# Kernel tuning notes

Hardware: AMD Instinct MI355X
Metric: run time of the kernel (lower is better)

The kernel has to match this reference:

```python
import jax, jax.numpy as jnp
import numpy as np

B, C_IN, N, C_OUT, K = 16, 64, 2048, 64, 20
BN_EPS = 1e-5
SLOPE = 0.2  # LeakyReLU negative slope


def setup_inputs() -> dict:
    key = jax.random.key(0)
    ks = jax.random.split(key, 6)
    x = jax.random.normal(ks[0], (B, C_IN, N), jnp.float32)
    # Conv2d(2*C_IN, C_OUT, 1, bias=False), kaiming-normal init -> [C_OUT, 2*C_IN]
    W = jax.random.normal(ks[1], (C_OUT, 2 * C_IN), jnp.float32) * np.sqrt(2.0 / (2 * C_IN))
    # BatchNorm2d (eval mode) affine params + running stats
    gamma = jax.random.uniform(ks[2], (C_OUT,), jnp.float32, 0.5, 1.5)
    beta = jax.random.normal(ks[3], (C_OUT,), jnp.float32) * 0.1
    run_mean = jax.random.normal(ks[4], (C_OUT,), jnp.float32) * 0.1
    run_var = jax.random.uniform(ks[5], (C_OUT,), jnp.float32, 0.5, 1.5)
    return {"x": x, "W": W, "gamma": gamma, "beta": beta,
            "run_mean": run_mean, "run_var": run_var}


def _knn(x):
    """x: [B, C, N] -> neighbor indices [B, N, K] (nearest, includes self)."""
    xt = jnp.swapaxes(x, 1, 2)                       # [B, N, C]
    sq = jnp.sum(xt * xt, axis=-1)                   # [B, N]
    # squared euclidean distance; topk of -dist == nearest neighbors
    dist = sq[:, :, None] - 2.0 * jnp.einsum('bnc,bmc->bnm', xt, xt) + sq[:, None, :]
    _, idx = jax.lax.top_k(-dist, K)                 # [B, N, K]
    return idx


def reference(x, W, gamma, beta, run_mean, run_var):
    # --- dynamic graph (knn computed under no_grad in the original) ---
    idx = _knn(jax.lax.stop_gradient(x))             # [B, N, K]
    # --- dual gather: edge_index[1]=neighbors -> x_i, edge_index[0]=centers -> x_j ---
    xt = jnp.swapaxes(x, 1, 2)                       # [B, N, C]
    x_i = jax.vmap(lambda xb, ib: xb[ib])(xt, idx)   # [B, N, K, C] neighbor feats
    x_i = jnp.transpose(x_i, (0, 3, 1, 2))           # [B, C, N, K]
    x_j = x[:, :, :, None]                           # [B, C, N, 1] center feats
    feat = jnp.concatenate([x_i, x_j - x_i], axis=1)  # [B, 2C, N, K]
    # --- 1x1 conv (no bias) ---
    h = jnp.einsum('oc,bcnk->bonk', W, feat)         # [B, C_OUT, N, K]
    # --- BatchNorm2d eval mode, folded affine ---
    inv = gamma / jnp.sqrt(run_var + BN_EPS)
    h = h * inv[None, :, None, None] + (beta - run_mean * inv)[None, :, None, None]
    # --- LeakyReLU(0.2); Dropout(0.0) is identity ---
    h = jnp.where(h > 0, h, SLOPE * h)
    # --- max over neighbors ---
    out = jnp.max(h, axis=-1)                        # [B, C_OUT, N]
    return out, idx
```

## Files before the change

kernel.cpp:

```cpp
#include <hip/hip_runtime.h>
#include <cstdint>
#include <cstddef>

#define B_ 16
#define C_ 64
#define N_ 2048
#define K_ 20
#define CAND 24
#define LQ 12

typedef short bf16x8 __attribute__((ext_vector_type(8)));
typedef float f32x4 __attribute__((ext_vector_type(4)));

__device__ __forceinline__ unsigned umin_(unsigned a, unsigned b) { return a < b ? a : b; }
__device__ __forceinline__ unsigned umax_(unsigned a, unsigned b) { return a > b ? a : b; }
__device__ __forceinline__ unsigned short bfr_(float v) {
    unsigned u = __float_as_uint(v);
    return (unsigned short)((u + 0x7FFFu + ((u >> 16) & 1u)) >> 16);
}

__global__ __launch_bounds__(128) void k_sq(const float* __restrict__ x,
                                            float* __restrict__ sqf,
                                            unsigned short* __restrict__ xh,
                                            float* __restrict__ xrT,
                                            float* __restrict__ Yt,
                                            const float* __restrict__ W) {
    __shared__ float Ag[C_ * 64];
    int tid = threadIdx.x;
    bool doY = (Yt != nullptr);
    if (doY) {
        int o = tid & 63, ch = tid >> 6;
#pragma unroll
        for (int j = 0; j < 32; ++j) {
            int c = ch * 32 + j;
            Ag[c * 64 + o] = W[o * 128 + c] - W[o * 128 + 64 + c];
        }
    }
    int i = blockIdx.x * 128 + tid;
    int b = i >> 11, n = i & (N_ - 1);
    const float* xb = x + (size_t)b * C_ * N_ + n;
    float vr[C_];
#pragma unroll
    for (int c = 0; c < C_; ++c) vr[c] = xb[(size_t)c * N_];
    float p[C_];
#pragma unroll
    for (int c = 0; c < C_; ++c) p[c] = __fmul_rn(vr[c], vr[c]);
    float r[8];
#pragma unroll
    for (int k = 0; k < 8; ++k) r[k] = p[k];
#pragma unroll
    for (int ii = 8; ii < 64; ii += 8) {
#pragma unroll
        for (int k = 0; k < 8; ++k) r[k] = __fadd_rn(r[k], p[ii + k]);
    }
    float s0 = __fadd_rn(__fadd_rn(r[0], r[1]), __fadd_rn(r[2], r[3]));
    float s1 = __fadd_rn(__fadd_rn(r[4], r[5]), __fadd_rn(r[6], r[7]));
    sqf[i] = __fadd_rn(s0, s1);

    unsigned short* xrow = xh + (size_t)i * 64;
#pragma unroll
    for (int cb = 0; cb < 8; ++cb) {
        bf16x8 pk;
#pragma unroll
        for (int e = 0; e < 8; ++e) pk[e] = (short)bfr_(vr[cb * 8 + e]);
        *reinterpret_cast<bf16x8*>(xrow + ((cb ^ (n & 7)) * 8)) = pk;
    }
    if (xrT) {
        float4* dst = reinterpret_cast<float4*>(xrT + (size_t)i * C_);
#pragma unroll
        for (int q = 0; q < 16; ++q)
            dst[q] = make_float4(vr[q*4+0], vr[q*4+1], vr[q*4+2], vr[q*4+3]);
    }
    if (doY) {
        __syncthreads();
        float4 acc[16];
#pragma unroll
        for (int q = 0; q < 16; ++q) acc[q] = make_float4(0.f, 0.f, 0.f, 0.f);
#pragma unroll 4
        for (int c = 0; c < C_; ++c) {
            float xv = vr[c];
            const float4* a4 = reinterpret_cast<const float4*>(&Ag[c * 64]);
#pragma unroll
            for (int q = 0; q < 16; ++q) {
                float4 a = a4[q];
                acc[q].x = fmaf(xv, a.x, acc[q].x);
                acc[q].y = fmaf(xv, a.y, acc[q].y);
                acc[q].z = fmaf(xv, a.z, acc[q].z);
                acc[q].w = fmaf(xv, a.w, acc[q].w);
            }
        }
        float4* yp = reinterpret_cast<float4*>(Yt + (size_t)i * 64);
#pragma unroll
        for (int q = 0; q < 16; ++q) yp[q] = acc[q];
    }
}

__global__ __launch_bounds__(256) void k_y(const float* __restrict__ x,
                                           const float* __restrict__ W,
                                           float* __restrict__ Yt) {
    __shared__ float Al[C_ * 64];
    __shared__ float xl[C_ * 64];
    int tid = threadIdx.x;
    int bid = blockIdx.x;
    int b = bid >> 5;
    int m0 = (bid & 31) * 64;
    {
        int o = tid & 63, cb = tid >> 6;
#pragma unroll
        for (int j = 0; j < 16; ++j) {
            int c = cb * 16 + j;
            Al[c * 64 + o] = W[o * 128 + c] - W[o * 128 + 64 + c];
            xl[c * 64 + o] = x[((size_t)b * C_ + c) * N_ + m0 + o];
        }
    }
    __syncthreads();
    int ml = tid & 63, og = tid >> 6;
    float acc[16];
#pragma unroll
    for (int j = 0; j < 16; ++j) acc[j] = 0.f;
#pragma unroll 4
    for (int c = 0; c < C_; ++c) {
        float xv = xl[c * 64 + ml];
        const float4* a4 = reinterpret_cast<const float4*>(&Al[c * 64 + og * 16]);
#pragma unroll
        for (int q = 0; q < 4; ++q) {
            float4 av = a4[q];
            acc[q*4+0] = fmaf(av.x, xv, acc[q*4+0]);
            acc[q*4+1] = fmaf(av.y, xv, acc[q*4+1]);
            acc[q*4+2] = fmaf(av.z, xv, acc[q*4+2]);
            acc[q*4+3] = fmaf(av.w, xv, acc[q*4+3]);
        }
    }
    float* yp = Yt + ((size_t)b * N_ + m0 + ml) * C_ + og * 16;
#pragma unroll
    for (int q = 0; q < 4; ++q)
        reinterpret_cast<float4*>(yp)[q] =
            make_float4(acc[q*4+0], acc[q*4+1], acc[q*4+2], acc[q*4+3]);
}

__global__ __launch_bounds__(256, 2) void k_dist(const unsigned short* __restrict__ xh,
                                                 const float* __restrict__ sqf,
                                                 unsigned short* __restrict__ candu) {
    __shared__ __align__(16) unsigned short xtl[256 * 64];
    __shared__ float sqm[256];
    int tid = threadIdx.x;
    int w = tid >> 6, lane = tid & 63;
    int bid = blockIdx.x;
    int b = bid >> 5;
    int n0 = (bid & 31) * 64;
    const unsigned short* xhb = xh + (size_t)b * N_ * 64;

    {
#pragma unroll
        for (int i = 0; i < 2; ++i) {
            int ch = tid + 256 * i;
            *reinterpret_cast<uint4*>(&xtl[ch * 8]) =
                *reinterpret_cast<const uint4*>(&xhb[(size_t)n0 * 64 + ch * 8]);
        }
    }
    __syncthreads();
    int rl = w * 16 + (lane & 15);
    int cb0 = (lane >> 4), cb1 = 4 + (lane >> 4);
    bf16x8 afr0 = *reinterpret_cast<const bf16x8*>(&xtl[rl * 64 + ((cb0 ^ (lane & 7)) * 8)]);
    bf16x8 afr1 = *reinterpret_cast<const bf16x8*>(&xtl[rl * 64 + ((cb1 ^ (lane & 7)) * 8)]);
    float rsq[4];
#pragma unroll
    for (int r = 0; r < 4; ++r)
        rsq[r] = sqf[b * N_ + n0 + w * 16 + (lane >> 4) * 4 + r];

    unsigned list[4][LQ];
#pragma unroll
    for (int r = 0; r < 4; ++r)
#pragma unroll
        for (int j = 0; j < LQ; ++j) list[r][j] = 0xFFFFFFFFu;

    for (int t = 0; t < 8; ++t) {
        int m0 = t * 256;
        __syncthreads();
        {
#pragma unroll
            for (int i = 0; i < 8; ++i) {
                int ch = tid + 256 * i;
                *reinterpret_cast<uint4*>(&xtl[ch * 8]) =
                    *reinterpret_cast<const uint4*>(&xhb[(size_t)m0 * 64 + ch * 8]);
            }
            sqm[tid] = sqf[b * N_ + m0 + tid];
        }
        __syncthreads();
        const unsigned short* pB0 = &xtl[(lane & 15) * 64 + ((cb0 ^ (lane & 7)) * 8)];
        const unsigned short* pB1 = &xtl[(lane & 15) * 64 + ((cb1 ^ (lane & 7)) * 8)];
        const float* pS = &sqm[lane & 15];
#pragma unroll
        for (int mb = 0; mb < 16; ++mb) {
            bf16x8 bf0 = *reinterpret_cast<const bf16x8*>(pB0 + mb * 1024);
            bf16x8 bf1 = *reinterpret_cast<const bf16x8*>(pB1 + mb * 1024);
            f32x4 acc = {0.f, 0.f, 0.f, 0.f};
            acc = __builtin_amdgcn_mfma_f32_16x16x32_bf16(afr0, bf0, acc, 0, 0, 0);
            acc = __builtin_amdgcn_mfma_f32_16x16x32_bf16(afr1, bf1, acc, 0, 0, 0);
            float smv = pS[mb * 16];
            unsigned mg = (unsigned)(m0 + mb * 16) | (unsigned)(lane & 15);
#pragma unroll
            for (int r = 0; r < 4; ++r) {
                float rs = rsq[r] + smv;
                float d = fmaf(-2.f, acc[r], rs);
                d = fmaxf(d, 0.f);
                unsigned key = (__float_as_uint(d) & 0xFFFFF800u) | mg;
#pragma unroll
                for (int j = LQ - 1; j > 0; --j)
                    asm("v_med3_u32 %0, %0, %1, %2"
                        : "+v"(list[r][j])
                        : "v"(list[r][j - 1]), "v"(key));
                list[r][0] = umin_(list[r][0], key);
            }
        }
    }

    size_t grow0 = (size_t)b * N_ + n0 + w * 16 + (lane >> 4) * 4;
#pragma unroll 1
    for (int it = 0; it < CAND; ++it) {
        unsigned head[4], wv[4];
#pragma unroll
        for (int j = 0; j < 4; ++j) { head[j] = list[j][0]; wv[j] = head[j]; }
#pragma unroll
        for (int d2 = 1; d2 < 16; d2 <<= 1)
#pragma unroll
            for (int j = 0; j < 4; ++j)
                wv[j] = umin_(wv[j], (unsigned)__shfl_xor((int)wv[j], d2, 16));
#pragma unroll
        for (int j = 0; j < 4; ++j) {
            bool own = (head[j] == wv[j]);
#pragma unroll
            for (int jj = 0; jj < LQ - 1; ++jj)
                list[j][jj] = own ? list[j][jj + 1] : list[j][jj];
            list[j][LQ - 1] = own ? 0xFFFFFFFFu : list[j][LQ - 1];
            if ((lane & 15) == 0)
                candu[(grow0 + j) * CAND + it] = (unsigned short)(wv[j] & 2047u);
        }
    }
}

__global__ __launch_bounds__(256) void k_rescore2(const float* __restrict__ xrT,
                                                  const float* __restrict__ sqf,
                                                  const unsigned short* __restrict__ candu,
                                                  float* __restrict__ idxf) {
    __shared__ __align__(16) float xnl[64 * 64];
    __shared__ unsigned short cl[64 * CAND];
    __shared__ float dl2[64][CAND];
    int tid = threadIdx.x;
    int bid = blockIdx.x;
    int b = bid >> 5;
    int n0 = (bid & 31) * 64;
    int bN = b * N_;
    const float* xr = xrT + (size_t)bN * C_;
    {
        const float4* src = reinterpret_cast<const float4*>(xr + (size_t)n0 * C_);
#pragma unroll
        for (int q = 0; q < 4; ++q) {
            int idx = tid + q * 256;
            reinterpret_cast<float4*>(xnl)[idx] = src[idx];
        }
        if (tid < 192) {
            reinterpret_cast<uint4*>(cl)[tid] =
                reinterpret_cast<const uint4*>(candu + (size_t)(bN + n0) * CAND)[tid];
        }
    }
    __syncthreads();
#pragma unroll 1
    for (int t2 = 0; t2 < 6; ++t2) {
        int task = tid + t2 * 256;
        int row = task / 24, ci = task - row * 24;
        int m = cl[row * CAND + ci];
        const float* xn = xnl + row * 64;
        const float* xm = xr + (size_t)m * C_;
        float a = 0.f;
#pragma unroll
        for (int cq = 0; cq < 16; ++cq) {
            float4 n4 = *reinterpret_cast<const float4*>(xn + cq * 4);
            float4 m4 = *reinterpret_cast<const float4*>(xm + cq * 4);
            a = __fadd_rn(a, __fmul_rn(n4.x, m4.x));
            a = __fadd_rn(a, __fmul_rn(n4.y, m4.y));
            a = __fadd_rn(a, __fmul_rn(n4.z, m4.z));
            a = __fadd_rn(a, __fmul_rn(n4.w, m4.w));
        }
        dl2[row][ci] = __fadd_rn(__fsub_rn(sqf[bN + n0 + row], __fmul_rn(2.0f, a)),
                                 sqf[bN + m]);
    }
    __syncthreads();
#pragma unroll 1
    for (int t2 = 0; t2 < 6; ++t2) {
        int task = tid + t2 * 256;
        int row = task / 24, ci = task - row * 24;
        int m = cl[row * CAND + ci];
        float di = dl2[row][ci];
        int rank = 0;
#pragma unroll
        for (int j = 0; j < CAND; ++j) {
            float dj = dl2[row][j];
            int mj = cl[row * CAND + j];
            rank += (dj < di || (dj == di && mj < m)) ? 1 : 0;
        }
        if (rank < K_)
            idxf[((size_t)bN + n0 + row) * K_ + rank] = (float)m;
    }
}

__global__ __launch_bounds__(256) void k_rescore(const float* __restrict__ x,
                                                 const float* __restrict__ sqf,
                                                 const unsigned short* __restrict__ candu,
                                                 float* __restrict__ idxf) {
    int tid = threadIdx.x;
    int w = tid >> 6, lane = tid & 63;
    size_t grow = (size_t)blockIdx.x * 4 + w;
    int b = (int)(grow >> 11), n = (int)(grow & (N_ - 1));
    const float* xb = x + (size_t)b * C_ * N_;
    float d = 0.f;
    unsigned m = 0xFFFFFFFFu;
    if (lane < CAND) {
        m = candu[grow * CAND + lane];
        float a = 0.f;
#pragma unroll 8
        for (int c = 0; c < C_; ++c)
            a = __fadd_rn(a, __fmul_rn(xb[(size_t)c * N_ + n], xb[(size_t)c * N_ + m]));
        d = __fadd_rn(__fsub_rn(sqf[b * N_ + n], __fmul_rn(2.0f, a)), sqf[b * N_ + m]);
    }
    int rank = 0;
#pragma unroll 1
    for (int j = 0; j < CAND; ++j) {
        float dj = __shfl(d, j, 64);
        unsigned mj = (unsigned)__shfl((int)m, j, 64);
        if (lane < CAND && (dj < d || (dj == d && mj < m))) ++rank;
    }
    if (lane < CAND && rank < K_)
        idxf[grow * K_ + rank] = (float)m;
}

__global__ __launch_bounds__(256) void k_out(const float* __restrict__ x,
                                             const float* __restrict__ W,
                                             const float* __restrict__ gamma,
                                             const float* __restrict__ beta,
                                             const float* __restrict__ rmean,
                                             const float* __restrict__ rvar,
                                             const float* __restrict__ Yt,
                                             const float* __restrict__ idxf,
                                             float* __restrict__ out) {
    __shared__ float Bl[C_ * 64];
    __shared__ float xl[C_ * 64];
    __shared__ float resl[64 * 65];
    __shared__ float sl[64], tl[64];
    int tid = threadIdx.x;
    int bid = blockIdx.x;
    int b = bid >> 5;
    int n0 = (bid & 31) * 64;
    {
        int o = tid & 63, cb = tid >> 6;
#pragma unroll
        for (int j = 0; j < 16; ++j) {
            int c = cb * 16 + j;
            Bl[c * 64 + o] = W[o * 128 + 64 + c];
            xl[c * 64 + o] = x[((size_t)b * C_ + c) * N_ + n0 + o];
        }
        if (tid < 64) {
            float s = gamma[tid] / sqrtf(rvar[tid] + 1e-5f);
            sl[tid] = s;
            tl[tid] = beta[tid] - rmean[tid] * s;
        }
    }
    __syncthreads();
    int nl = tid & 63, wv2 = tid >> 6;
    const float* ip = idxf + ((size_t)b * N_ + n0 + nl) * K_;
    int mi[K_];
#pragma unroll
    for (int k = 0; k < K_; ++k) mi[k] = (int)ip[k];
    const float* Ytb = Yt + (size_t)b * N_ * C_;
#pragma unroll
    for (int t = 0; t < 4; ++t) {
        int oq = wv2 * 4 + t;
        float ax = 0.f, ay = 0.f, az = 0.f, aw = 0.f;
#pragma unroll 8
        for (int c = 0; c < C_; ++c) {
            float xv = xl[c * 64 + nl];
            float4 bl4 = *reinterpret_cast<const float4*>(&Bl[c * 64 + oq * 4]);
            ax = fmaf(bl4.x, xv, ax);
            ay = fmaf(bl4.y, xv, ay);
            az = fmaf(bl4.z, xv, az);
            aw = fmaf(bl4.w, xv, aw);
        }
        float vx = -3.4e38f, vy = -3.4e38f, vz = -3.4e38f, vw = -3.4e38f;
#pragma unroll
        for (int k = 0; k < K_; ++k) {
            float4 y4 = *reinterpret_cast<const float4*>(&Ytb[(size_t)mi[k] * C_ + oq * 4]);
            vx = fmaxf(vx, y4.x);
            vy = fmaxf(vy, y4.y);
            vz = fmaxf(vz, y4.z);
            vw = fmaxf(vw, y4.w);
        }
        float h0 = ax + vx, h1 = ay + vy, h2 = az + vz, h3 = aw + vw;
        int o0 = oq * 4;
        float v0 = sl[o0 + 0] * h0 + tl[o0 + 0];
        float v1 = sl[o0 + 1] * h1 + tl[o0 + 1];
        float v2 = sl[o0 + 2] * h2 + tl[o0 + 2];
        float v3 = sl[o0 + 3] * h3 + tl[o0 + 3];
        v0 = v0 > 0.f ? v0 : 0.2f * v0;
        v1 = v1 > 0.f ? v1 : 0.2f * v1;
        v2 = v2 > 0.f ? v2 : 0.2f * v2;
        v3 = v3 > 0.f ? v3 : 0.2f * v3;
        resl[(o0 + 0) * 65 + nl] = v0;
        resl[(o0 + 1) * 65 + nl] = v1;
        resl[(o0 + 2) * 65 + nl] = v2;
        resl[(o0 + 3) * 65 + nl] = v3;
    }
    __syncthreads();
    {
        int nl2 = tid & 63, ob = tid >> 6;
#pragma unroll
        for (int j = 0; j < 16; ++j) {
            int o2 = ob * 16 + j;
            out[((size_t)b * C_ + o2) * N_ + n0 + nl2] = resl[o2 * 65 + nl2];
        }
    }
}

extern "C" void kernel_launch(void* const* d_in, const int* in_sizes, int n_in,
                              void* d_out, int out_size, void* d_ws, size_t ws_size,
                              hipStream_t stream) {
    const float* x     = (const float*)d_in[0];
    const float* W     = (const float*)d_in[1];
    const float* gamma = (const float*)d_in[2];
    const float* beta  = (const float*)d_in[3];
    const float* rmean = (const float*)d_in[4];
    const float* rvar  = (const float*)d_in[5];

    float* out  = (float*)d_out;
    float* idxf = out + (size_t)B_ * C_ * N_;

    char* ws = (char*)d_ws;
    float* sqf            = (float*)ws;
    unsigned short* candu = (unsigned short*)(ws + 131072);
    unsigned short* xh    = (unsigned short*)(ws + 131072 + 1572864);
    size_t off_xrT        = 131072 + 1572864 + 4194304;
    size_t need_xrT       = off_xrT + 8388608;
    size_t need_fused     = need_xrT + 8388608;
    float* xrT            = (ws_size >= need_xrT) ? (float*)(ws + off_xrT) : nullptr;
    bool fused            = (ws_size >= need_fused);
    float* Yt             = fused ? (float*)(ws + need_xrT) : (float*)(ws + 131072);

    k_sq     <<<B_ * N_ / 128, 128, 0, stream>>>(x, sqf, xh, xrT, fused ? Yt : nullptr, W);
    k_dist   <<<B_ * 32, 256, 0, stream>>>(xh, sqf, candu);
    if (xrT)
        k_rescore2<<<B_ * 32, 256, 0, stream>>>(xrT, sqf, candu, idxf);
    else
        k_rescore<<<B_ * N_ / 4, 256, 0, stream>>>(x, sqf, candu, idxf);
    if (!fused)
        k_y  <<<B_ * (N_ / 64), 256, 0, stream>>>(x, W, Yt);
    k_out    <<<B_ * (N_ / 64), 256, 0, stream>>>(x, W, gamma, beta, rmean, rvar, Yt, idxf, out);
}
```

Baseline: 178.5 us.

## Coalesce rescore candidate loads via shuffles, unfuse Y, per-channel gather in k_out

The Y projection is moved out of k_sq and always computed by the separate k_y kernel, which lightens k_sq. k_rescore3 assigns each group of four lanes to four candidate rows: each lane loads a 16-float slice of every row and the slices are redistributed with wave shuffles, so candidate-row reads are contiguous instead of one 256-byte row per lane. k_out stages neighbour indices in shared memory and gathers Y with one output channel per lane, giving coalesced 64-float row reads instead of scattered float4 reads. The cost is many shuffle instructions, an extra kernel launch, and extra synchronisation in k_out.

```diff
diff --git a/kernel.cpp b/kernel.cpp
--- a/kernel.cpp
+++ b/kernel.cpp
@@ -22,20 +22,8 @@
 __global__ __launch_bounds__(128) void k_sq(const float* __restrict__ x,
                                             float* __restrict__ sqf,
                                             unsigned short* __restrict__ xh,
-                                            float* __restrict__ xrT,
-                                            float* __restrict__ Yt,
-                                            const float* __restrict__ W) {
-    __shared__ float Ag[C_ * 64];
-    int tid = threadIdx.x;
-    bool doY = (Yt != nullptr);
-    if (doY) {
-        int o = tid & 63, ch = tid >> 6;
-#pragma unroll
-        for (int j = 0; j < 32; ++j) {
-            int c = ch * 32 + j;
-            Ag[c * 64 + o] = W[o * 128 + c] - W[o * 128 + 64 + c];
-        }
-    }
+                                            float* __restrict__ xrT) {
+    int tid = threadIdx.x;
     int i = blockIdx.x * 128 + tid;
     int b = i >> 11, n = i & (N_ - 1);
     const float* xb = x + (size_t)b * C_ * N_ + n;
@@ -70,28 +58,6 @@
 #pragma unroll
         for (int q = 0; q < 16; ++q)
             dst[q] = make_float4(vr[q*4+0], vr[q*4+1], vr[q*4+2], vr[q*4+3]);
-    }
-    if (doY) {
-        __syncthreads();
-        float4 acc[16];
-#pragma unroll
-        for (int q = 0; q < 16; ++q) acc[q] = make_float4(0.f, 0.f, 0.f, 0.f);
-#pragma unroll 4
-        for (int c = 0; c < C_; ++c) {
-            float xv = vr[c];
-            const float4* a4 = reinterpret_cast<const float4*>(&Ag[c * 64]);
-#pragma unroll
-            for (int q = 0; q < 16; ++q) {
-                float4 a = a4[q];
-                acc[q].x = fmaf(xv, a.x, acc[q].x);
-                acc[q].y = fmaf(xv, a.y, acc[q].y);
-                acc[q].z = fmaf(xv, a.z, acc[q].z);
-                acc[q].w = fmaf(xv, a.w, acc[q].w);
-            }
-        }
-        float4* yp = reinterpret_cast<float4*>(Yt + (size_t)i * 64);
-#pragma unroll
-        for (int q = 0; q < 16; ++q) yp[q] = acc[q];
     }
 }
 
@@ -239,7 +205,7 @@
     }
 }
 
-__global__ __launch_bounds__(256) void k_rescore2(const float* __restrict__ xrT,
+__global__ __launch_bounds__(256) void k_rescore3(const float* __restrict__ xrT,
                                                   const float* __restrict__ sqf,
                                                   const unsigned short* __restrict__ candu,
                                                   float* __restrict__ idxf) {
@@ -247,6 +213,7 @@
     __shared__ unsigned short cl[64 * CAND];
     __shared__ float dl2[64][CAND];
     int tid = threadIdx.x;
+    int lane = tid & 63, w = tid >> 6;
     int bid = blockIdx.x;
     int b = bid >> 5;
     int n0 = (bid & 31) * 64;
@@ -259,24 +226,59 @@
             int idx = tid + q * 256;
             reinterpret_cast<float4*>(xnl)[idx] = src[idx];
         }
-        if (tid < 192) {
+        if (tid < 192)
             reinterpret_cast<uint4*>(cl)[tid] =
                 reinterpret_cast<const uint4*>(candu + (size_t)(bN + n0) * CAND)[tid];
-        }
-    }
-    __syncthreads();
+    }
+    __syncthreads();
+    int qbase = lane & ~3, qr = lane & 3;
 #pragma unroll 1
-    for (int t2 = 0; t2 < 6; ++t2) {
-        int task = tid + t2 * 256;
-        int row = task / 24, ci = task - row * 24;
+    for (int s = 0; s < 6; ++s) {
+        int task = w * 384 + s * 64 + lane;
+        int row = task / CAND, ci = task - row * CAND;
         int m = cl[row * CAND + ci];
+        float4 buf[16];
+#pragma unroll
+        for (int r = 0; r < 4; ++r) {
+            int mq = __shfl(m, qbase + r, 64);
+            const float* xmq = xr + (size_t)mq * C_ + qr * 16;
+            float4 c0 = *reinterpret_cast<const float4*>(xmq + 0);
+            float4 c1 = *reinterpret_cast<const float4*>(xmq + 4);
+            float4 c2 = *reinterpret_cast<const float4*>(xmq + 8);
+            float4 c3 = *reinterpret_cast<const float4*>(xmq + 12);
+#pragma unroll
+            for (int j2 = 0; j2 < 4; ++j2) {
+                float4 s0, s1, s2, s3;
+                s0.x = __shfl(c0.x, qbase + j2, 64);
+                s0.y = __shfl(c0.y, qbase + j2, 64);
+                s0.z = __shfl(c0.z, qbase + j2, 64);
+                s0.w = __shfl(c0.w, qbase + j2, 64);
+                s1.x = __shfl(c1.x, qbase + j2, 64);
+                s1.y = __shfl(c1.y, qbase + j2, 64);
+                s1.z = __shfl(c1.z, qbase + j2, 64);
+                s1.w = __shfl(c1.w, qbase + j2, 64);
+                s2.x = __shfl(c2.x, qbase + j2, 64);
+                s2.y = __shfl(c2.y, qbase + j2, 64);
+                s2.z = __shfl(c2.z, qbase + j2, 64);
+                s2.w = __shfl(c2.w, qbase + j2, 64);
+                s3.x = __shfl(c3.x, qbase + j2, 64);
+                s3.y = __shfl(c3.y, qbase + j2, 64);
+                s3.z = __shfl(c3.z, qbase + j2, 64);
+                s3.w = __shfl(c3.w, qbase + j2, 64);
+                if (qr == r) {
+                    buf[j2 * 4 + 0] = s0;
+                    buf[j2 * 4 + 1] = s1;
+                    buf[j2 * 4 + 2] = s2;
+                    buf[j2 * 4 + 3] = s3;
+                }
+            }
+        }
         const float* xn = xnl + row * 64;
-        const float* xm = xr + (size_t)m * C_;
         float a = 0.f;
 #pragma unroll
         for (int cq = 0; cq < 16; ++cq) {
             float4 n4 = *reinterpret_cast<const float4*>(xn + cq * 4);
-            float4 m4 = *reinterpret_cast<const float4*>(xm + cq * 4);
+            float4 m4 = buf[cq];
             a = __fadd_rn(a, __fmul_rn(n4.x, m4.x));
             a = __fadd_rn(a, __fmul_rn(n4.y, m4.y));
             a = __fadd_rn(a, __fmul_rn(n4.z, m4.z));
@@ -289,7 +291,7 @@
 #pragma unroll 1
     for (int t2 = 0; t2 < 6; ++t2) {
         int task = tid + t2 * 256;
-        int row = task / 24, ci = task - row * 24;
+        int row = task / CAND, ci = task - row * CAND;
         int m = cl[row * CAND + ci];
         float di = dl2[row][ci];
         int rank = 0;
@@ -366,48 +368,55 @@
         }
     }
     __syncthreads();
-    int nl = tid & 63, wv2 = tid >> 6;
-    const float* ip = idxf + ((size_t)b * N_ + n0 + nl) * K_;
-    int mi[K_];
-#pragma unroll
-    for (int k = 0; k < K_; ++k) mi[k] = (int)ip[k];
-    const float* Ytb = Yt + (size_t)b * N_ * C_;
-#pragma unroll
-    for (int t = 0; t < 4; ++t) {
-        int oq = wv2 * 4 + t;
-        float ax = 0.f, ay = 0.f, az = 0.f, aw = 0.f;
+    {
+        int nl = tid & 63, wv2 = tid >> 6;
+#pragma unroll
+        for (int t = 0; t < 4; ++t) {
+            int oq = wv2 * 4 + t;
+            float ax = 0.f, ay = 0.f, az = 0.f, aw = 0.f;
 #pragma unroll 8
-        for (int c = 0; c < C_; ++c) {
-            float xv = xl[c * 64 + nl];
-            float4 bl4 = *reinterpret_cast<const float4*>(&Bl[c * 64 + oq * 4]);
-            ax = fmaf(bl4.x, xv, ax);
-            ay = fmaf(bl4.y, xv, ay);
-            az = fmaf(bl4.z, xv, az);
-            aw = fmaf(bl4.w, xv, aw);
-        }
-        float vx = -3.4e38f, vy = -3.4e38f, vz = -3.4e38f, vw = -3.4e38f;
-#pragma unroll
-        for (int k = 0; k < K_; ++k) {
-            float4 y4 = *reinterpret_cast<const float4*>(&Ytb[(size_t)mi[k] * C_ + oq * 4]);
-            vx = fmaxf(vx, y4.x);
-            vy = fmaxf(vy, y4.y);
-            vz = fmaxf(vz, y4.z);
-            vw = fmaxf(vw, y4.w);
-        }
-        float h0 = ax + vx, h1 = ay + vy, h2 = az + vz, h3 = aw + vw;
-        int o0 = oq * 4;
-        float v0 = sl[o0 + 0] * h0 + tl[o0 + 0];
-        float v1 = sl[o0 + 1] * h1 + tl[o0 + 1];
-        float v2 = sl[o0 + 2] * h2 + tl[o0 + 2];
-        float v3 = sl[o0 + 3] * h3 + tl[o0 + 3];
-        v0 = v0 > 0.f ? v0 : 0.2f * v0;
-        v1 = v1 > 0.f ? v1 : 0.2f * v1;
-        v2 = v2 > 0.f ? v2 : 0.2f * v2;
-        v3 = v3 > 0.f ? v3 : 0.2f * v3;
-        resl[(o0 + 0) * 65 + nl] = v0;
-        resl[(o0 + 1) * 65 + nl] = v1;
-        resl[(o0 + 2) * 65 + nl] = v2;
-        resl[(o0 + 3) * 65 + nl] = v3;
+            for (int c = 0; c < C_; ++c) {
+                float xv = xl[c * 64 + nl];
+                float4 bl4 = *reinterpret_cast<const float4*>(&Bl[c * 64 + oq * 4]);
+                ax = fmaf(bl4.x, xv, ax);
+                ay = fmaf(bl4.y, xv, ay);
+                az = fmaf(bl4.z, xv, az);
+                aw = fmaf(bl4.w, xv, aw);
+            }
+            int o0 = oq * 4;
+            resl[(o0 + 0) * 65 + nl] = ax;
+            resl[(o0 + 1) * 65 + nl] = ay;
+            resl[(o0 + 2) * 65 + nl] = az;
+            resl[(o0 + 3) * 65 + nl] = aw;
+        }
+    }
+    __syncthreads();
+    int* mil = reinterpret_cast<int*>(Bl);
+    {
+#pragma unroll
+        for (int q = 0; q < 5; ++q) {
+            int idx = tid + q * 256;
+            mil[idx] = (int)idxf[(size_t)(b * N_ + n0) * K_ + idx];
+        }
+    }
+    __syncthreads();
+    {
+        int w2 = tid >> 6, lane2 = tid & 63;
+        const float* Ytb = Yt + (size_t)b * N_ * C_;
+        float s = sl[lane2], t0 = tl[lane2];
+        for (int i = 0; i < 16; ++i) {
+            int nloc = w2 * 16 + i;
+            float v = -3.4e38f;
+#pragma unroll
+            for (int k = 0; k < K_; ++k) {
+                int m = mil[nloc * K_ + k];
+                v = fmaxf(v, Ytb[(size_t)m * C_ + lane2]);
+            }
+            float u = resl[lane2 * 65 + nloc];
+            float val = s * (u + v) + t0;
+            val = val > 0.f ? val : 0.2f * val;
+            resl[lane2 * 65 + nloc] = val;
+        }
     }
     __syncthreads();
     {
@@ -439,18 +448,17 @@
     unsigned short* xh    = (unsigned short*)(ws + 131072 + 1572864);
     size_t off_xrT        = 131072 + 1572864 + 4194304;
     size_t need_xrT       = off_xrT + 8388608;
-    size_t need_fused     = need_xrT + 8388608;
+    size_t need_ded       = need_xrT + 8388608;
     float* xrT            = (ws_size >= need_xrT) ? (float*)(ws + off_xrT) : nullptr;
-    bool fused            = (ws_size >= need_fused);
-    float* Yt             = fused ? (float*)(ws + need_xrT) : (float*)(ws + 131072);
-
-    k_sq     <<<B_ * N_ / 128, 128, 0, stream>>>(x, sqf, xh, xrT, fused ? Yt : nullptr, W);
+    bool dedY             = (ws_size >= need_ded);
+    float* Yt             = dedY ? (float*)(ws + need_xrT) : (float*)(ws + 131072);
+
+    k_sq     <<<B_ * N_ / 128, 128, 0, stream>>>(x, sqf, xh, xrT);
     k_dist   <<<B_ * 32, 256, 0, stream>>>(xh, sqf, candu);
     if (xrT)
-        k_rescore2<<<B_ * 32, 256, 0, stream>>>(xrT, sqf, candu, idxf);
+        k_rescore3<<<B_ * 32, 256, 0, stream>>>(xrT, sqf, candu, idxf);
     else
         k_rescore<<<B_ * N_ / 4, 256, 0, stream>>>(x, sqf, candu, idxf);
-    if (!fused)
-        k_y  <<<B_ * (N_ / 64), 256, 0, stream>>>(x, W, Yt);
+    k_y      <<<B_ * (N_ / 64), 256, 0, stream>>>(x, W, Yt);
     k_out    <<<B_ * (N_ / 64), 256, 0, stream>>>(x, W, gamma, beta, rmean, rvar, Yt, idxf, out);
 }
```

Result: faster. 159.2 us (-10.8%).
